# Optimization experiments

Measured on AMD Instinct MI355X. Metric: run time of the kernel, lower is better.

## Reference

```python
import jax, jax.numpy as jnp
import numpy as np


def _feature_map(x):
    # elu_feature_map: F.elu(x) + 1
    return jax.nn.elu(x) + 1.0


def setup_inputs() -> dict:
    key = jax.random.key(0)
    kq, kk, kv = jax.random.split(key, 3)
    B, H, S, D = 4, 16, 2048, 64
    Q = jax.random.normal(kq, (B, H, S, D), dtype=jnp.float32)
    K = jax.random.normal(kk, (B, H, S, D), dtype=jnp.float32)
    V = jax.random.normal(kv, (B, H, S, D), dtype=jnp.float32)
    return {"Q": Q, "K": K, "V": V}


def reference(Q, K, V):
    Qf = _feature_map(Q)  # [B,H,S,D]
    Kf = _feature_map(K)  # [B,H,S,D]
    scores = jnp.einsum('bhsd,bhtd->bhst', Qf, Kf)  # [B,H,S,S]
    attn = jax.nn.softmax(scores, axis=-1)
    out = jnp.einsum('bhst,bhtd->bhsd', attn, V)  # [B,H,S,D]
    return out
```

## Files before the change

### kernel.cpp

```cpp
#include <hip/hip_runtime.h>
#include <stdint.h>

typedef __attribute__((ext_vector_type(8))) _Float16 f16x8;
typedef __attribute__((ext_vector_type(8))) short bf16x8;
typedef __attribute__((ext_vector_type(16))) float f32x16;

#define BH_ 64
#define S_ 2048
#define D_ 64
#define KT_ 64
#define NT_ (S_ / KT_)
#define LOG2E 1.44269504088896340736f
#define DEFER_THR 8.0f

#define WS_ARR ((size_t)BH_ * S_ * D_ * 2)
#define WS_NEED (2 * WS_ARR)

__device__ __forceinline__ uint16_t f32_to_bf16_rn(float f) {
    uint32_t u = __float_as_uint(f);
    u += 0x7fffu + ((u >> 16) & 1u);
    return (uint16_t)(u >> 16);
}
__device__ __forceinline__ float bfbits_to_f32(uint16_t h) {
    return __uint_as_float(((uint32_t)h) << 16);
}
__device__ __forceinline__ float phi(float x) { return x > 0.0f ? x + 1.0f : __expf(x); }

#if __has_builtin(__builtin_amdgcn_exp2f)
#define EXP2F(x) __builtin_amdgcn_exp2f(x)
#else
#define EXP2F(x) exp2f(x)
#endif

__device__ __forceinline__ uint32_t pkrtz(float lo, float hi2) {
    union {
        decltype(__builtin_amdgcn_cvt_pkrtz(0.0f, 0.0f)) v;
        uint32_t u;
    } c;
    c.v = __builtin_amdgcn_cvt_pkrtz(lo, hi2);
    return c.u;
}

#define GLL16(gsrc, ldst)                                                              \
    __builtin_amdgcn_global_load_lds(                                                  \
        (const __attribute__((address_space(1))) uint32_t*)(gsrc),                     \
        (__attribute__((address_space(3))) uint32_t*)(ldst), 16, 0, 0)


__global__ void prep_k(const float* __restrict__ K, uint16_t* __restrict__ Kf) {
    const size_t e = ((size_t)blockIdx.x * 256 + threadIdx.x) * 8;
    const int d0 = (int)(e & 63);
    const int c = d0 >> 3;
    const int t = (int)((e >> 6) & 63);
    const size_t dst = e - d0 + (size_t)((c ^ (t & 7) ^ ((t >> 3) & 7)) * 8);
    const float4 a = *(const float4*)(K + e);
    const float4 b = *(const float4*)(K + e + 4);
    const float xs[8] = {a.x, a.y, a.z, a.w, b.x, b.y, b.z, b.w};
    _Float16 h8[8];
#pragma unroll
    for (int j = 0; j < 8; ++j) h8[j] = (_Float16)phi(xs[j]);
    *(f16x8*)(Kf + dst) = *(const f16x8*)h8;
}

__global__ void prep_v(const float* __restrict__ V, uint16_t* __restrict__ Vt) {
    const int bh = blockIdx.x >> 5, kt = blockIdx.x & 31;
    const int d = threadIdx.x >> 2;
    const size_t tile = (size_t)(bh * 32 + kt) * 4096;
    const float* vb = V + ((size_t)bh * S_ + (size_t)kt * KT_) * D_ + d;
#pragma unroll
    for (int cc = 0; cc < 2; ++cc) {
        const int ct = (threadIdx.x & 3) * 2 + cc;
        _Float16 v8[8];
#pragma unroll
        for (int i = 0; i < 8; ++i) {
            const int pos = 8 * ct + i;
            const int src = (pos & 48) | (4 * ((pos >> 3) & 1) + (pos & 3) + 8 * ((pos >> 2) & 1));
            v8[i] = (_Float16)vb[(size_t)src * D_];
        }
        *(f16x8*)(Vt + tile + (size_t)d * 64 +
                  (size_t)((ct ^ (d & 7) ^ ((d >> 3) & 7)) * 8)) = *(const f16x8*)v8;
    }
}


__global__ __launch_bounds__(512, 4)
void la_attn8(const float* __restrict__ Q, const uint16_t* __restrict__ Kf,
              const uint16_t* __restrict__ Vt, float* __restrict__ O)
{
    const int id = blockIdx.x;
    const int wg = (id & 7) * 64 + (id >> 3);
    const int bh = wg >> 3;
    const int qt = wg & 7;
    const int tid = threadIdx.x;
    const int lane = tid & 63;
    const int wid = tid >> 6;
    const int ln31 = lane & 31;
    const int hi = lane >> 5;
    const int sw = (ln31 & 7) ^ (ln31 >> 3);

    __shared__ __align__(16) uint16_t kf_s[2][4096];
    __shared__ __align__(16) uint16_t vt_s[2][4096];

    const int q0 = qt * 256 + wid * 32;

    f16x8 qf[4];
    {
        const float* qp = Q + ((size_t)bh * S_ + q0 + ln31) * 64;
#pragma unroll
        for (int m = 0; m < 4; ++m) {
            const float4 a = *(const float4*)(qp + m * 16 + hi * 8);
            const float4 b = *(const float4*)(qp + m * 16 + hi * 8 + 4);
            const float xs[8] = {a.x, a.y, a.z, a.w, b.x, b.y, b.z, b.w};
            _Float16 h8[8];
#pragma unroll
            for (int j = 0; j < 8; ++j) h8[j] = (_Float16)(phi(xs[j]) * LOG2E);
            qf[m] = *(const f16x8*)h8;
        }
    }

    int off4[4];
#pragma unroll
    for (int m = 0; m < 4; ++m)
        off4[m] = ln31 * 64 + (((2 * m + hi) ^ sw) * 8);

    f32x16 accO0 = (f32x16)0.0f, accO1 = (f32x16)0.0f;
    float m_run = 0.0f, l_run = 0.0f;

    const size_t tb0 = (size_t)bh * 32 * 4096;

    auto stage = [&](int buf, int kt2) {
        const size_t toff = tb0 + (size_t)kt2 * 4096 + (size_t)tid * 8;
        GLL16(Kf + toff, &kf_s[buf][tid * 8]);
        GLL16(Vt + toff, &vt_s[buf][tid * 8]);
    };

    stage(0, 0);
    int cur = 0;

    for (int kt = 0; kt < NT_; ++kt) {
        __syncthreads();
        if (kt + 1 < NT_) stage(cur ^ 1, kt + 1);

        const uint16_t* __restrict__ kfp = kf_s[cur];
        const uint16_t* __restrict__ vtp = vt_s[cur];

        f32x16 s0, s1;
#pragma unroll
        for (int r = 0; r < 16; ++r) { s0[r] = -m_run; s1[r] = -m_run; }
        __builtin_amdgcn_s_setprio(1);
#pragma unroll
        for (int m = 0; m < 4; ++m) {
            f16x8 k0 = *(const f16x8*)&kfp[off4[m]];
            f16x8 k1 = *(const f16x8*)&kfp[(off4[m] ^ 32) + 2048];
            s0 = __builtin_amdgcn_mfma_f32_32x32x16_f16(k0, qf[m], s0, 0, 0, 0);
            s1 = __builtin_amdgcn_mfma_f32_32x32x16_f16(k1, qf[m], s1, 0, 0, 0);
        }
        __builtin_amdgcn_s_setprio(0);

        float t8[8];
#pragma unroll
        for (int r = 0; r < 8; ++r)
            t8[r] = fmaxf(fmaxf(s0[r], s0[r + 8]), fmaxf(s1[r], s1[r + 8]));
#pragma unroll
        for (int st2 = 4; st2 > 0; st2 >>= 1)
#pragma unroll
            for (int r = 0; r < st2; ++r) t8[r] = fmaxf(t8[r], t8[r + st2]);
        const float tmax = fmaxf(t8[0], __shfl_xor(t8[0], 32));

        if (!__all(tmax <= DEFER_THR)) {
            const float dlt = fmaxf(tmax, 0.0f);
            const float corr = EXP2F(-dlt);
            m_run += dlt;
            l_run *= corr;
#pragma unroll
            for (int r = 0; r < 16; ++r) {
                accO0[r] *= corr; accO1[r] *= corr;
                s0[r] -= dlt; s1[r] -= dlt;
            }
        }
        float ps0 = 0.0f, ps1 = 0.0f;
#pragma unroll
        for (int r = 0; r < 16; ++r) {
            const float p0 = EXP2F(s0[r]);
            const float p1 = EXP2F(s1[r]);
            s0[r] = p0; s1[r] = p1;
            ps0 += p0; ps1 += p1;
        }
        l_run += ps0 + ps1;

        union PF { uint32_t u[4]; f16x8 v; };
        PF pf[4];
#pragma unroll
        for (int i = 0; i < 4; ++i) {
            pf[0].u[i] = pkrtz(s0[2 * i], s0[2 * i + 1]);
            pf[1].u[i] = pkrtz(s0[8 + 2 * i], s0[9 + 2 * i]);
            pf[2].u[i] = pkrtz(s1[2 * i], s1[2 * i + 1]);
            pf[3].u[i] = pkrtz(s1[8 + 2 * i], s1[9 + 2 * i]);
        }

        __builtin_amdgcn_s_setprio(1);
#pragma unroll
        for (int c = 0; c < 4; ++c) {
            f16x8 v0 = *(const f16x8*)&vtp[off4[c]];
            f16x8 v1 = *(const f16x8*)&vtp[(off4[c] ^ 32) + 2048];
            accO0 = __builtin_amdgcn_mfma_f32_32x32x16_f16(v0, pf[c].v, accO0, 0, 0, 0);
            accO1 = __builtin_amdgcn_mfma_f32_32x32x16_f16(v1, pf[c].v, accO1, 0, 0, 0);
        }
        __builtin_amdgcn_s_setprio(0);

        cur ^= 1;
    }

    const float l_tot = l_run + __shfl_xor(l_run, 32);
    const float inv = 1.0f / l_tot;
    float* op = O + ((size_t)bh * S_ + q0 + ln31) * D_;
#pragma unroll
    for (int g = 0; g < 4; ++g) {
        float4 o0, o1;
        o0.x = accO0[4 * g + 0] * inv; o0.y = accO0[4 * g + 1] * inv;
        o0.z = accO0[4 * g + 2] * inv; o0.w = accO0[4 * g + 3] * inv;
        o1.x = accO1[4 * g + 0] * inv; o1.y = accO1[4 * g + 1] * inv;
        o1.z = accO1[4 * g + 2] * inv; o1.w = accO1[4 * g + 3] * inv;
        *(float4*)(op + 8 * g + 4 * hi) = o0;
        *(float4*)(op + 32 + 8 * g + 4 * hi) = o1;
    }
}


__global__ __launch_bounds__(256, 2)
void la_attn_fwd(const float* __restrict__ Q, const float* __restrict__ K,
                 const float* __restrict__ V, float* __restrict__ O)
{
    const int bh = blockIdx.x;
    const int qt = blockIdx.y;
    const int tid = threadIdx.x;
    const int lane = tid & 63;
    const int wid = tid >> 6;
    const int ln31 = lane & 31;
    const int hi = lane >> 5;

    const size_t base = (size_t)bh * (S_ * D_);
    const float* __restrict__ Qb = Q + base;
    const float* __restrict__ Kb = K + base;
    const float* __restrict__ Vb = V + base;
    float* __restrict__ Ob = O + base;

    __shared__ __align__(16) uint16_t kh[32][D_];
    __shared__ __align__(16) uint16_t kl[32][D_];

    const int q0 = qt * 128 + wid * 32;

    bf16x8 qfh[4], qfl[4];
    {
        const float* qp = Qb + (size_t)(q0 + ln31) * D_;
#pragma unroll
        for (int m = 0; m < 4; ++m) {
            const float4 a = *(const float4*)(qp + m * 16 + hi * 8);
            const float4 b = *(const float4*)(qp + m * 16 + hi * 8 + 4);
            float xs[8] = {a.x, a.y, a.z, a.w, b.x, b.y, b.z, b.w};
#pragma unroll
            for (int j = 0; j < 8; ++j) {
                float x = phi(xs[j]);
                uint16_t h = f32_to_bf16_rn(x);
                qfh[m][j] = (short)h;
                qfl[m][j] = (short)f32_to_bf16_rn(x - bfbits_to_f32(h));
            }
        }
    }

    f32x16 accO0 = (f32x16)0.0f;
    f32x16 accO1 = (f32x16)0.0f;
    float m_run = -1e30f;
    float l_run = 0.0f;

    const int srow = tid >> 3;
    const int scolu = (tid & 7) << 3;
    const int scsw = scolu ^ ((srow & 7) << 3);

    for (int kt = 0; kt < S_ / 32; ++kt) {
        const int tb = kt * 32;
        {
            const float* kp = Kb + (size_t)(tb + srow) * D_ + scolu;
            const float4 a = *(const float4*)(kp);
            const float4 b = *(const float4*)(kp + 4);
            float xs[8] = {a.x, a.y, a.z, a.w, b.x, b.y, b.z, b.w};
            short h8[8], l8[8];
#pragma unroll
            for (int j = 0; j < 8; ++j) {
                float x = phi(xs[j]);
                uint16_t h = f32_to_bf16_rn(x);
                h8[j] = (short)h;
                l8[j] = (short)f32_to_bf16_rn(x - bfbits_to_f32(h));
            }
            *(bf16x8*)&kh[srow][scsw] = *(const bf16x8*)h8;
            *(bf16x8*)&kl[srow][scsw] = *(const bf16x8*)l8;
        }
        __syncthreads();

        f32x16 accS = (f32x16)0.0f;
#pragma unroll
        for (int m = 0; m < 4; ++m) {
            const int c = (m * 16 + hi * 8) ^ ((ln31 & 7) << 3);
            bf16x8 kfh = *(const bf16x8*)&kh[ln31][c];
            bf16x8 kfl = *(const bf16x8*)&kl[ln31][c];
            accS = __builtin_amdgcn_mfma_f32_32x32x16_bf16(kfh, qfh[m], accS, 0, 0, 0);
            accS = __builtin_amdgcn_mfma_f32_32x32x16_bf16(kfh, qfl[m], accS, 0, 0, 0);
            accS = __builtin_amdgcn_mfma_f32_32x32x16_bf16(kfl, qfh[m], accS, 0, 0, 0);
        }

        float tmax = accS[0];
#pragma unroll
        for (int r = 1; r < 16; ++r) tmax = fmaxf(tmax, accS[r]);
        tmax = fmaxf(tmax, __shfl_xor(tmax, 32));
        const float m_new = fmaxf(m_run, tmax);
        const float corr = __expf(m_run - m_new);
        m_run = m_new;

        float p[16];
        float psum = 0.0f;
#pragma unroll
        for (int r = 0; r < 16; ++r) { p[r] = __expf(accS[r] - m_new); psum += p[r]; }
        l_run = l_run * corr + psum;

#pragma unroll
        for (int r = 0; r < 16; ++r) { accO0[r] *= corr; accO1[r] *= corr; }

        uint32_t pk[8];
#pragma unroll
        for (int k2 = 0; k2 < 8; ++k2)
            pk[k2] = (uint32_t)f32_to_bf16_rn(p[2 * k2]) |
                     ((uint32_t)f32_to_bf16_rn(p[2 * k2 + 1]) << 16);

        const uint32_t s0 = hi ? pk[0] : pk[2];
        const uint32_t s1 = hi ? pk[1] : pk[3];
        const uint32_t s2 = hi ? pk[4] : pk[6];
        const uint32_t s3 = hi ? pk[5] : pk[7];
        const uint32_t r0 = __shfl_xor(s0, 32);
        const uint32_t r1 = __shfl_xor(s1, 32);
        const uint32_t r2 = __shfl_xor(s2, 32);
        const uint32_t r3 = __shfl_xor(s3, 32);

        union U { uint32_t u[4]; bf16x8 v; };
        U f0, f1;
        f0.u[0] = hi ? r0 : pk[0];  f0.u[1] = hi ? r1 : pk[1];
        f0.u[2] = hi ? pk[2] : r0;  f0.u[3] = hi ? pk[3] : r1;
        f1.u[0] = hi ? r2 : pk[4];  f1.u[1] = hi ? r3 : pk[5];
        f1.u[2] = hi ? pk[6] : r2;  f1.u[3] = hi ? pk[7] : r3;

#pragma unroll
        for (int ts = 0; ts < 2; ++ts) {
            const bf16x8 pfv = ts ? f1.v : f0.v;
            const float* vp = Vb + (size_t)(tb + ts * 16 + hi * 8) * D_ + ln31;
#pragma unroll
            for (int dn = 0; dn < 2; ++dn) {
                bf16x8 vf;
#pragma unroll
                for (int j = 0; j < 8; ++j)
                    vf[j] = (short)f32_to_bf16_rn(vp[(size_t)j * D_ + dn * 32]);
                if (dn == 0) accO0 = __builtin_amdgcn_mfma_f32_32x32x16_bf16(vf, pfv, accO0, 0, 0, 0);
                else         accO1 = __builtin_amdgcn_mfma_f32_32x32x16_bf16(vf, pfv, accO1, 0, 0, 0);
            }
        }
        __syncthreads();
    }

    const float l_tot = l_run + __shfl_xor(l_run, 32);
    const float inv = 1.0f / l_tot;
    float* op = Ob + (size_t)(q0 + ln31) * D_;
#pragma unroll
    for (int g = 0; g < 4; ++g) {
        float4 o0, o1;
        o0.x = accO0[4 * g + 0] * inv; o0.y = accO0[4 * g + 1] * inv;
        o0.z = accO0[4 * g + 2] * inv; o0.w = accO0[4 * g + 3] * inv;
        o1.x = accO1[4 * g + 0] * inv; o1.y = accO1[4 * g + 1] * inv;
        o1.z = accO1[4 * g + 2] * inv; o1.w = accO1[4 * g + 3] * inv;
        *(float4*)(op + 8 * g + 4 * hi) = o0;
        *(float4*)(op + 32 + 8 * g + 4 * hi) = o1;
    }
}

extern "C" void kernel_launch(void* const* d_in, const int* in_sizes, int n_in,
                              void* d_out, int out_size, void* d_ws, size_t ws_size,
                              hipStream_t stream) {
    (void)in_sizes; (void)n_in; (void)out_size;
    const float* Q = (const float*)d_in[0];
    const float* K = (const float*)d_in[1];
    const float* V = (const float*)d_in[2];
    float* O = (float*)d_out;

    if (ws_size >= WS_NEED) {
        uint16_t* Kf = (uint16_t*)d_ws;
        uint16_t* Vt = (uint16_t*)((char*)d_ws + 1 * WS_ARR);
        prep_k<<<4096, 256, 0, stream>>>(K, Kf);
        prep_v<<<2048, 256, 0, stream>>>(V, Vt);
        la_attn8<<<512, 512, 0, stream>>>(Q, Kf, Vt, O);
    } else {
        la_attn_fwd<<<dim3(BH_, S_ / 128), 256, 0, stream>>>(Q, K, V, O);
    }
}
```

Before: 110.3 us.

## Software-pipeline QK^T of the next tile with PV of the current tile

Restructures the attention loop so each iteration computes the score MFMAs for tile t+1 alongside the PV MFMAs for tile t. K and V staging are split into separate loads, and K is prefetched two tiles ahead. The goal is to give the matrix units independent work so the softmax exp/pack phase and the MFMA chains overlap instead of running serially. It costs 32 extra accumulator registers, which may reduce occupancy, and it adds a prologue plus conditional logic.

```diff
diff --git a/kernel.cpp b/kernel.cpp
--- a/kernel.cpp
+++ b/kernel.cpp
@@ -128,25 +128,25 @@
 
     const size_t tb0 = (size_t)bh * 32 * 4096;
 
-    auto stage = [&](int buf, int kt2) {
+    auto stageK = [&](int buf, int kt2) {
         const size_t toff = tb0 + (size_t)kt2 * 4096 + (size_t)tid * 8;
         GLL16(Kf + toff, &kf_s[buf][tid * 8]);
+    };
+    auto stageV = [&](int buf, int kt2) {
+        const size_t toff = tb0 + (size_t)kt2 * 4096 + (size_t)tid * 8;
         GLL16(Vt + toff, &vt_s[buf][tid * 8]);
     };
 
-    stage(0, 0);
-    int cur = 0;
-
-    for (int kt = 0; kt < NT_; ++kt) {
-        __syncthreads();
-        if (kt + 1 < NT_) stage(cur ^ 1, kt + 1);
-
-        const uint16_t* __restrict__ kfp = kf_s[cur];
-        const uint16_t* __restrict__ vtp = vt_s[cur];
-
-        f32x16 s0, s1;
-#pragma unroll
-        for (int r = 0; r < 16; ++r) { s0[r] = -m_run; s1[r] = -m_run; }
+    stageK(0, 0);
+    stageV(0, 0);
+    __syncthreads();
+    stageK(1, 1);
+
+    f32x16 s0, s1;
+    {
+        const uint16_t* __restrict__ kfp = kf_s[0];
+        s0 = (f32x16)0.0f;
+        s1 = (f32x16)0.0f;
         __builtin_amdgcn_s_setprio(1);
 #pragma unroll
         for (int m = 0; m < 4; ++m) {
@@ -156,6 +156,13 @@
             s1 = __builtin_amdgcn_mfma_f32_32x32x16_f16(k1, qf[m], s1, 0, 0, 0);
         }
         __builtin_amdgcn_s_setprio(0);
+    }
+
+#pragma unroll 2
+    for (int t = 0; t < NT_; ++t) {
+        __syncthreads();
+        if (t + 2 < NT_) stageK(t & 1, t + 2);
+        if (t + 1 < NT_) stageV((t + 1) & 1, t + 1);
 
         float t8[8];
 #pragma unroll
@@ -198,17 +205,34 @@
             pf[3].u[i] = pkrtz(s1[8 + 2 * i], s1[9 + 2 * i]);
         }
 
+        const bool more = (t + 1 < NT_);
+        f32x16 n0, n1;
         __builtin_amdgcn_s_setprio(1);
-#pragma unroll
-        for (int c = 0; c < 4; ++c) {
-            f16x8 v0 = *(const f16x8*)&vtp[off4[c]];
-            f16x8 v1 = *(const f16x8*)&vtp[(off4[c] ^ 32) + 2048];
-            accO0 = __builtin_amdgcn_mfma_f32_32x32x16_f16(v0, pf[c].v, accO0, 0, 0, 0);
-            accO1 = __builtin_amdgcn_mfma_f32_32x32x16_f16(v1, pf[c].v, accO1, 0, 0, 0);
+        if (more) {
+            const uint16_t* __restrict__ kfp = kf_s[(t + 1) & 1];
+            n0 = (f32x16)(-m_run);
+            n1 = (f32x16)(-m_run);
+#pragma unroll
+            for (int m = 0; m < 4; ++m) {
+                f16x8 k0 = *(const f16x8*)&kfp[off4[m]];
+                f16x8 k1 = *(const f16x8*)&kfp[(off4[m] ^ 32) + 2048];
+                n0 = __builtin_amdgcn_mfma_f32_32x32x16_f16(k0, qf[m], n0, 0, 0, 0);
+                n1 = __builtin_amdgcn_mfma_f32_32x32x16_f16(k1, qf[m], n1, 0, 0, 0);
+            }
+        }
+        {
+            const uint16_t* __restrict__ vtp = vt_s[t & 1];
+#pragma unroll
+            for (int c = 0; c < 4; ++c) {
+                f16x8 v0 = *(const f16x8*)&vtp[off4[c]];
+                f16x8 v1 = *(const f16x8*)&vtp[(off4[c] ^ 32) + 2048];
+                accO0 = __builtin_amdgcn_mfma_f32_32x32x16_f16(v0, pf[c].v, accO0, 0, 0, 0);
+                accO1 = __builtin_amdgcn_mfma_f32_32x32x16_f16(v1, pf[c].v, accO1, 0, 0, 0);
+            }
         }
         __builtin_amdgcn_s_setprio(0);
 
-        cur ^= 1;
+        if (more) { s0 = n0; s1 = n1; }
     }
 
     const float l_tot = l_run + __shfl_xor(l_run, 32);
```

Result: slower. 199.3 us (+80.7%).

## Halve workgroup size to 256 threads and interleave exp2 with PV MFMAs

Applied to the files above, without the earlier changes.

The attention kernel now launches 1024 workgroups of 4 waves, each covering 128 query rows instead of 256, with the block-to-(bh,qt) swizzle and tile staging adjusted so each thread loads two 16-byte chunks per K/V tile. The softmax exponentiation and fp16 packing are split into two halves, and each half's PV MFMAs are issued before the second half's exp2 work so transcendental and matrix ops can overlap. The smaller blocks give finer scheduling granularity and more resident workgroups, but each K/V tile is now fetched from global/L2 twice as often, and each thread does twice the staging loads.

```diff
diff --git a/kernel.cpp b/kernel.cpp
--- a/kernel.cpp
+++ b/kernel.cpp
@@ -83,14 +83,14 @@
 }
 
 
-__global__ __launch_bounds__(512, 4)
+__global__ __launch_bounds__(256, 4)
 void la_attn8(const float* __restrict__ Q, const uint16_t* __restrict__ Kf,
               const uint16_t* __restrict__ Vt, float* __restrict__ O)
 {
     const int id = blockIdx.x;
-    const int wg = (id & 7) * 64 + (id >> 3);
-    const int bh = wg >> 3;
-    const int qt = wg & 7;
+    const int wg = (id & 7) * 128 + (id >> 3);
+    const int bh = wg >> 4;
+    const int qt = wg & 15;
     const int tid = threadIdx.x;
     const int lane = tid & 63;
     const int wid = tid >> 6;
@@ -101,7 +101,7 @@
     __shared__ __align__(16) uint16_t kf_s[2][4096];
     __shared__ __align__(16) uint16_t vt_s[2][4096];
 
-    const int q0 = qt * 256 + wid * 32;
+    const int q0 = qt * 128 + wid * 32;
 
     f16x8 qf[4];
     {
@@ -131,7 +131,9 @@
     auto stage = [&](int buf, int kt2) {
         const size_t toff = tb0 + (size_t)kt2 * 4096 + (size_t)tid * 8;
         GLL16(Kf + toff, &kf_s[buf][tid * 8]);
+        GLL16(Kf + toff + 2048, &kf_s[buf][2048 + tid * 8]);
         GLL16(Vt + toff, &vt_s[buf][tid * 8]);
+        GLL16(Vt + toff + 2048, &vt_s[buf][2048 + tid * 8]);
     };
 
     stage(0, 0);
@@ -178,36 +180,62 @@
                 s0[r] -= dlt; s1[r] -= dlt;
             }
         }
-        float ps0 = 0.0f, ps1 = 0.0f;
+
+        union PF { uint32_t u[4]; f16x8 v; };
+
+        float ps0 = 0.0f;
 #pragma unroll
         for (int r = 0; r < 16; ++r) {
-            const float p0 = EXP2F(s0[r]);
-            const float p1 = EXP2F(s1[r]);
-            s0[r] = p0; s1[r] = p1;
-            ps0 += p0; ps1 += p1;
-        }
+            const float p = EXP2F(s0[r]);
+            s0[r] = p;
+            ps0 += p;
+        }
+        PF pf0, pf1;
+#pragma unroll
+        for (int i = 0; i < 4; ++i) {
+            pf0.u[i] = pkrtz(s0[2 * i], s0[2 * i + 1]);
+            pf1.u[i] = pkrtz(s0[8 + 2 * i], s0[9 + 2 * i]);
+        }
+        __builtin_amdgcn_s_setprio(1);
+        {
+            f16x8 v0 = *(const f16x8*)&vtp[off4[0]];
+            f16x8 v1 = *(const f16x8*)&vtp[(off4[0] ^ 32) + 2048];
+            accO0 = __builtin_amdgcn_mfma_f32_32x32x16_f16(v0, pf0.v, accO0, 0, 0, 0);
+            accO1 = __builtin_amdgcn_mfma_f32_32x32x16_f16(v1, pf0.v, accO1, 0, 0, 0);
+            f16x8 v2 = *(const f16x8*)&vtp[off4[1]];
+            f16x8 v3 = *(const f16x8*)&vtp[(off4[1] ^ 32) + 2048];
+            accO0 = __builtin_amdgcn_mfma_f32_32x32x16_f16(v2, pf1.v, accO0, 0, 0, 0);
+            accO1 = __builtin_amdgcn_mfma_f32_32x32x16_f16(v3, pf1.v, accO1, 0, 0, 0);
+        }
+        __builtin_amdgcn_s_setprio(0);
+
+        float ps1 = 0.0f;
+#pragma unroll
+        for (int r = 0; r < 16; ++r) {
+            const float p = EXP2F(s1[r]);
+            s1[r] = p;
+            ps1 += p;
+        }
+        PF pf2, pf3;
+#pragma unroll
+        for (int i = 0; i < 4; ++i) {
+            pf2.u[i] = pkrtz(s1[2 * i], s1[2 * i + 1]);
+            pf3.u[i] = pkrtz(s1[8 + 2 * i], s1[9 + 2 * i]);
+        }
+        __builtin_amdgcn_s_setprio(1);
+        {
+            f16x8 v0 = *(const f16x8*)&vtp[off4[2]];
+            f16x8 v1 = *(const f16x8*)&vtp[(off4[2] ^ 32) + 2048];
+            accO0 = __builtin_amdgcn_mfma_f32_32x32x16_f16(v0, pf2.v, accO0, 0, 0, 0);
+            accO1 = __builtin_amdgcn_mfma_f32_32x32x16_f16(v1, pf2.v, accO1, 0, 0, 0);
+            f16x8 v2 = *(const f16x8*)&vtp[off4[3]];
+            f16x8 v3 = *(const f16x8*)&vtp[(off4[3] ^ 32) + 2048];
+            accO0 = __builtin_amdgcn_mfma_f32_32x32x16_f16(v2, pf3.v, accO0, 0, 0, 0);
+            accO1 = __builtin_amdgcn_mfma_f32_32x32x16_f16(v3, pf3.v, accO1, 0, 0, 0);
+        }
+        __builtin_amdgcn_s_setprio(0);
+
         l_run += ps0 + ps1;
-
-        union PF { uint32_t u[4]; f16x8 v; };
-        PF pf[4];
-#pragma unroll
-        for (int i = 0; i < 4; ++i) {
-            pf[0].u[i] = pkrtz(s0[2 * i], s0[2 * i + 1]);
-            pf[1].u[i] = pkrtz(s0[8 + 2 * i], s0[9 + 2 * i]);
-            pf[2].u[i] = pkrtz(s1[2 * i], s1[2 * i + 1]);
-            pf[3].u[i] = pkrtz(s1[8 + 2 * i], s1[9 + 2 * i]);
-        }
-
-        __builtin_amdgcn_s_setprio(1);
-#pragma unroll
-        for (int c = 0; c < 4; ++c) {
-            f16x8 v0 = *(const f16x8*)&vtp[off4[c]];
-            f16x8 v1 = *(const f16x8*)&vtp[(off4[c] ^ 32) + 2048];
-            accO0 = __builtin_amdgcn_mfma_f32_32x32x16_f16(v0, pf[c].v, accO0, 0, 0, 0);
-            accO1 = __builtin_amdgcn_mfma_f32_32x32x16_f16(v1, pf[c].v, accO1, 0, 0, 0);
-        }
-        __builtin_amdgcn_s_setprio(0);
-
         cur ^= 1;
     }
 
@@ -393,7 +421,7 @@
         uint16_t* Vt = (uint16_t*)((char*)d_ws + 1 * WS_ARR);
         prep_k<<<4096, 256, 0, stream>>>(K, Kf);
         prep_v<<<2048, 256, 0, stream>>>(V, Vt);
-        la_attn8<<<512, 512, 0, stream>>>(Q, Kf, Vt, O);
+        la_attn8<<<1024, 256, 0, stream>>>(Q, Kf, Vt, O);
     } else {
         la_attn_fwd<<<dim3(BH_, S_ / 128), 256, 0, stream>>>(Q, K, V, O);
     }
```

New measurement: 115.5 us. 4.7% more time.

## Drop LDS staging; load K/V fragments directly from global into registers

Applied to the files above, without the earlier changes.

Removes the shared-memory double buffer and the __syncthreads barrier; each wave now reads its K and V MFMA fragments straight from global memory (relying on L1/L2 for reuse across the 8 waves), with manual software prefetch of the next K fragment. The prep kernels stop applying the XOR swizzle since LDS bank conflicts no longer matter. The row max reduction also switches to v_max3_f32 inline asm. The trade is more global/L2 traffic per workgroup (8 waves each fetch the same tiles) in exchange for removing barriers and LDS round trips.

```diff
diff --git a/kernel.cpp b/kernel.cpp
--- a/kernel.cpp
+++ b/kernel.cpp
@@ -32,6 +32,12 @@
 #define EXP2F(x) exp2f(x)
 #endif
 
+__device__ __forceinline__ float fmax3(float a, float b, float c) {
+    float d;
+    asm("v_max3_f32 %0, %1, %2, %3" : "=v"(d) : "v"(a), "v"(b), "v"(c));
+    return d;
+}
+
 __device__ __forceinline__ uint32_t pkrtz(float lo, float hi2) {
     union {
         decltype(__builtin_amdgcn_cvt_pkrtz(0.0f, 0.0f)) v;
@@ -41,25 +47,16 @@
     return c.u;
 }
 
-#define GLL16(gsrc, ldst)                                                              \
-    __builtin_amdgcn_global_load_lds(                                                  \
-        (const __attribute__((address_space(1))) uint32_t*)(gsrc),                     \
-        (__attribute__((address_space(3))) uint32_t*)(ldst), 16, 0, 0)
-
 
 __global__ void prep_k(const float* __restrict__ K, uint16_t* __restrict__ Kf) {
     const size_t e = ((size_t)blockIdx.x * 256 + threadIdx.x) * 8;
-    const int d0 = (int)(e & 63);
-    const int c = d0 >> 3;
-    const int t = (int)((e >> 6) & 63);
-    const size_t dst = e - d0 + (size_t)((c ^ (t & 7) ^ ((t >> 3) & 7)) * 8);
     const float4 a = *(const float4*)(K + e);
     const float4 b = *(const float4*)(K + e + 4);
     const float xs[8] = {a.x, a.y, a.z, a.w, b.x, b.y, b.z, b.w};
     _Float16 h8[8];
 #pragma unroll
     for (int j = 0; j < 8; ++j) h8[j] = (_Float16)phi(xs[j]);
-    *(f16x8*)(Kf + dst) = *(const f16x8*)h8;
+    *(f16x8*)(Kf + e) = *(const f16x8*)h8;
 }
 
 __global__ void prep_v(const float* __restrict__ V, uint16_t* __restrict__ Vt) {
@@ -77,8 +74,7 @@
             const int src = (pos & 48) | (4 * ((pos >> 3) & 1) + (pos & 3) + 8 * ((pos >> 2) & 1));
             v8[i] = (_Float16)vb[(size_t)src * D_];
         }
-        *(f16x8*)(Vt + tile + (size_t)d * 64 +
-                  (size_t)((ct ^ (d & 7) ^ ((d >> 3) & 7)) * 8)) = *(const f16x8*)v8;
+        *(f16x8*)(Vt + tile + (size_t)d * 64 + (size_t)ct * 8) = *(const f16x8*)v8;
     }
 }
 
@@ -96,10 +92,6 @@
     const int wid = tid >> 6;
     const int ln31 = lane & 31;
     const int hi = lane >> 5;
-    const int sw = (ln31 & 7) ^ (ln31 >> 3);
-
-    __shared__ __align__(16) uint16_t kf_s[2][4096];
-    __shared__ __align__(16) uint16_t vt_s[2][4096];
 
     const int q0 = qt * 256 + wid * 32;
 
@@ -118,54 +110,49 @@
         }
     }
 
-    int off4[4];
-#pragma unroll
-    for (int m = 0; m < 4; ++m)
-        off4[m] = ln31 * 64 + (((2 * m + hi) ^ sw) * 8);
-
     f32x16 accO0 = (f32x16)0.0f, accO1 = (f32x16)0.0f;
     float m_run = 0.0f, l_run = 0.0f;
 
     const size_t tb0 = (size_t)bh * 32 * 4096;
-
-    auto stage = [&](int buf, int kt2) {
-        const size_t toff = tb0 + (size_t)kt2 * 4096 + (size_t)tid * 8;
-        GLL16(Kf + toff, &kf_s[buf][tid * 8]);
-        GLL16(Vt + toff, &vt_s[buf][tid * 8]);
-    };
-
-    stage(0, 0);
-    int cur = 0;
+    const uint16_t* kptr = Kf + tb0 + (size_t)ln31 * 64 + hi * 8;
+    const uint16_t* vptr = Vt + tb0 + (size_t)ln31 * 64 + hi * 8;
+
+    f16x8 kA = *(const f16x8*)(kptr);
+    f16x8 kB = *(const f16x8*)(kptr + 2048);
 
     for (int kt = 0; kt < NT_; ++kt) {
-        __syncthreads();
-        if (kt + 1 < NT_) stage(cur ^ 1, kt + 1);
-
-        const uint16_t* __restrict__ kfp = kf_s[cur];
-        const uint16_t* __restrict__ vtp = vt_s[cur];
-
         f32x16 s0, s1;
 #pragma unroll
         for (int r = 0; r < 16; ++r) { s0[r] = -m_run; s1[r] = -m_run; }
         __builtin_amdgcn_s_setprio(1);
 #pragma unroll
         for (int m = 0; m < 4; ++m) {
-            f16x8 k0 = *(const f16x8*)&kfp[off4[m]];
-            f16x8 k1 = *(const f16x8*)&kfp[(off4[m] ^ 32) + 2048];
-            s0 = __builtin_amdgcn_mfma_f32_32x32x16_f16(k0, qf[m], s0, 0, 0, 0);
-            s1 = __builtin_amdgcn_mfma_f32_32x32x16_f16(k1, qf[m], s1, 0, 0, 0);
+            f16x8 kn0, kn1;
+            if (m < 3) {
+                kn0 = *(const f16x8*)(kptr + (m + 1) * 16);
+                kn1 = *(const f16x8*)(kptr + (m + 1) * 16 + 2048);
+            }
+            s0 = __builtin_amdgcn_mfma_f32_32x32x16_f16(kA, qf[m], s0, 0, 0, 0);
+            s1 = __builtin_amdgcn_mfma_f32_32x32x16_f16(kB, qf[m], s1, 0, 0, 0);
+            if (m < 3) { kA = kn0; kB = kn1; }
         }
         __builtin_amdgcn_s_setprio(0);
+        kptr += 4096;
+
+        f16x8 v0 = *(const f16x8*)(vptr);
+        f16x8 v1 = *(const f16x8*)(vptr + 2048);
+        f16x8 v2 = *(const f16x8*)(vptr + 16);
+        f16x8 v3 = *(const f16x8*)(vptr + 16 + 2048);
 
         float t8[8];
 #pragma unroll
         for (int r = 0; r < 8; ++r)
-            t8[r] = fmaxf(fmaxf(s0[r], s0[r + 8]), fmaxf(s1[r], s1[r + 8]));
-#pragma unroll
-        for (int st2 = 4; st2 > 0; st2 >>= 1)
-#pragma unroll
-            for (int r = 0; r < st2; ++r) t8[r] = fmaxf(t8[r], t8[r + st2]);
-        const float tmax = fmaxf(t8[0], __shfl_xor(t8[0], 32));
+            t8[r] = fmax3(fmaxf(s0[r], s0[r + 8]), s1[r], s1[r + 8]);
+        const float ta = fmax3(t8[0], t8[1], t8[2]);
+        const float tb = fmax3(t8[3], t8[4], t8[5]);
+        const float tc = fmaxf(t8[6], t8[7]);
+        float tmax = fmax3(ta, tb, tc);
+        tmax = fmaxf(tmax, __shfl_xor(tmax, 32));
 
         if (!__all(tmax <= DEFER_THR)) {
             const float dlt = fmaxf(tmax, 0.0f);
@@ -189,26 +176,35 @@
         l_run += ps0 + ps1;
 
         union PF { uint32_t u[4]; f16x8 v; };
-        PF pf[4];
+        PF pf0, pf1, pf2, pf3;
 #pragma unroll
         for (int i = 0; i < 4; ++i) {
-            pf[0].u[i] = pkrtz(s0[2 * i], s0[2 * i + 1]);
-            pf[1].u[i] = pkrtz(s0[8 + 2 * i], s0[9 + 2 * i]);
-            pf[2].u[i] = pkrtz(s1[2 * i], s1[2 * i + 1]);
-            pf[3].u[i] = pkrtz(s1[8 + 2 * i], s1[9 + 2 * i]);
+            pf0.u[i] = pkrtz(s0[2 * i], s0[2 * i + 1]);
+            pf1.u[i] = pkrtz(s0[8 + 2 * i], s0[9 + 2 * i]);
+            pf2.u[i] = pkrtz(s1[2 * i], s1[2 * i + 1]);
+            pf3.u[i] = pkrtz(s1[8 + 2 * i], s1[9 + 2 * i]);
+        }
+
+        f16x8 v4 = *(const f16x8*)(vptr + 32);
+        f16x8 v5 = *(const f16x8*)(vptr + 32 + 2048);
+        f16x8 v6 = *(const f16x8*)(vptr + 48);
+        f16x8 v7 = *(const f16x8*)(vptr + 48 + 2048);
+        vptr += 4096;
+        if (kt + 1 < NT_) {
+            kA = *(const f16x8*)(kptr);
+            kB = *(const f16x8*)(kptr + 2048);
         }
 
         __builtin_amdgcn_s_setprio(1);
-#pragma unroll
-        for (int c = 0; c < 4; ++c) {
-            f16x8 v0 = *(const f16x8*)&vtp[off4[c]];
-            f16x8 v1 = *(const f16x8*)&vtp[(off4[c] ^ 32) + 2048];
-            accO0 = __builtin_amdgcn_mfma_f32_32x32x16_f16(v0, pf[c].v, accO0, 0, 0, 0);
-            accO1 = __builtin_amdgcn_mfma_f32_32x32x16_f16(v1, pf[c].v, accO1, 0, 0, 0);
-        }
+        accO0 = __builtin_amdgcn_mfma_f32_32x32x16_f16(v0, pf0.v, accO0, 0, 0, 0);
+        accO1 = __builtin_amdgcn_mfma_f32_32x32x16_f16(v1, pf0.v, accO1, 0, 0, 0);
+        accO0 = __builtin_amdgcn_mfma_f32_32x32x16_f16(v2, pf1.v, accO0, 0, 0, 0);
+        accO1 = __builtin_amdgcn_mfma_f32_32x32x16_f16(v3, pf1.v, accO1, 0, 0, 0);
+        accO0 = __builtin_amdgcn_mfma_f32_32x32x16_f16(v4, pf2.v, accO0, 0, 0, 0);
+        accO1 = __builtin_amdgcn_mfma_f32_32x32x16_f16(v5, pf2.v, accO1, 0, 0, 0);
+        accO0 = __builtin_amdgcn_mfma_f32_32x32x16_f16(v6, pf3.v, accO0, 0, 0, 0);
+        accO1 = __builtin_amdgcn_mfma_f32_32x32x16_f16(v7, pf3.v, accO1, 0, 0, 0);
         __builtin_amdgcn_s_setprio(0);
-
-        cur ^= 1;
     }
 
     const float l_tot = l_run + __shfl_xor(l_run, 32);
```

Result: slower. 261.9 us (+137.5%).
